# Optimization experiments

Measured on AMD Instinct MI355X. Metric: run time of the kernel, lower is better.

The kernel has to match this reference:

```python
import jax, jax.numpy as jnp
import numpy as np
import math

B, S, D_MODEL, H, D_LATENT = 2, 2048, 2048, 16, 512
D_HEAD = D_MODEL // H


def setup_inputs() -> dict:
    key = jax.random.key(0)
    ks = jax.random.split(key, 6)
    s = lambda fan: 1.0 / math.sqrt(fan)
    return {
        "x": jax.random.normal(ks[0], (B, S, D_MODEL), dtype=jnp.float32),
        "W_q": jax.random.normal(ks[1], (D_MODEL, D_MODEL), dtype=jnp.float32) * s(D_MODEL),
        "W_down_kv": jax.random.normal(ks[2], (D_LATENT, D_MODEL), dtype=jnp.float32) * s(D_MODEL),
        "W_up_k": jax.random.normal(ks[3], (H, D_HEAD, D_LATENT), dtype=jnp.float32) * s(D_LATENT),
        "W_up_v": jax.random.normal(ks[4], (H, D_HEAD, D_LATENT), dtype=jnp.float32) * s(D_LATENT),
        "W_o": jax.random.normal(ks[5], (D_MODEL, D_MODEL), dtype=jnp.float32) * s(D_MODEL),
    }


def reference(x, W_q, W_down_kv, W_up_k, W_up_v, W_o):
    b, s_len, d_model = x.shape
    # Q: (B, H, S, Dh)
    Q = (x @ W_q.T).reshape(b, s_len, H, D_HEAD).transpose(0, 2, 1, 3)
    # latent KV: (B, S, d_latent)
    C_kv = x @ W_down_kv.T
    # per-head up-projections fused into one einsum: (B, H, S, Dh)
    K = jnp.einsum("bsl,hdl->bhsd", C_kv, W_up_k)
    V = jnp.einsum("bsl,hdl->bhsd", C_kv, W_up_v)
    scores = jnp.einsum("bhsd,bhtd->bhst", Q, K) / math.sqrt(D_HEAD)
    attn = jax.nn.softmax(scores, axis=-1)  # dropout p=0 / eval -> identity
    out = jnp.einsum("bhst,bhtd->bhsd", attn, V)
    out = out.transpose(0, 2, 1, 3).reshape(b, s_len, H * D_HEAD)
    return out @ W_o.T
```

## Files before the change

### kernel.cpp

```cpp
#include <hip/hip_runtime.h>
#include <hip/hip_bf16.h>

typedef __hip_bfloat16 bf16;
typedef __attribute__((ext_vector_type(8))) short short8v;
typedef __attribute__((ext_vector_type(4))) short short4v;
typedef __attribute__((ext_vector_type(4))) float f32x4;

#define MFMA_16x16x32(a, b, c) __builtin_amdgcn_mfma_f32_16x16x32_bf16((a), (b), (c), 0, 0, 0)

constexpr int Bc = 2, Sc = 2048, DMc = 2048, Hc = 16, DLc = 512, DHc = 128;

__device__ __forceinline__ void gload_lds16(const bf16* g, void* lds) {
  __builtin_amdgcn_global_load_lds(
      (const __attribute__((address_space(1))) void*)g,
      (__attribute__((address_space(3))) void*)lds, 16, 0, 0);
}

__device__ __forceinline__ unsigned short bf16bits(float f) {
  return __builtin_bit_cast(unsigned short, __float2bfloat16(f));
}

struct CvtArgs {
  const float* src[6];
  bf16* dst[6];
  unsigned int cum[6];
  unsigned int total4;
};

__global__ __launch_bounds__(256) void cvt_all_kernel(CvtArgs a)
{
  unsigned int i = blockIdx.x * 256 + threadIdx.x;
  const unsigned int stride = gridDim.x * 256;
  for (; i < a.total4; i += stride) {
    int s = 0;
#pragma unroll
    for (int k = 1; k < 6; ++k) s += (i >= a.cum[k]) ? 1 : 0;
    unsigned int off = (i - a.cum[s]) * 4;
    float4 v = *(const float4*)(a.src[s] + off);
    short4v p;
    p[0] = (short)bf16bits(v.x);
    p[1] = (short)bf16bits(v.y);
    p[2] = (short)bf16bits(v.z);
    p[3] = (short)bf16bits(v.w);
    *(short4v*)(a.dst[s] + off) = p;
  }
}

template<int EPI>
__device__ __forceinline__ void gemm_tile_128(
    const bf16* __restrict__ A, const bf16* __restrict__ BT, void* __restrict__ Cv,
    int K, int ldc, int row0, int col0, bf16* As, bf16* Bs)
{
  const int tid = threadIdx.x;
  const int lane = tid & 63, wid = tid >> 6;
  const int wr = wid >> 1, wc = wid & 1;

  f32x4 acc[4][4] = {};

  const int srow = tid >> 2;
  const int scol = (tid & 3) * 8;
  const bf16* Ag = A + (size_t)(row0 + srow) * K + scol;
  const bf16* Bg = BT + (size_t)(col0 + srow) * K + scol;
  char* AsW = (char*)As + wid * 1024;
  char* BsW = (char*)Bs + wid * 1024;

  const int fr = lane & 15, fk = (lane >> 4) * 8;
  const bf16* aRd = As + (wr * 64 + fr) * 32 + fk;
  const bf16* bRd = Bs + (wc * 64 + fr) * 32 + fk;

  for (int k0 = 0; k0 < K; k0 += 32) {
    gload_lds16(Ag, AsW);
    gload_lds16(Ag + (size_t)64 * K, AsW + 4096);
    gload_lds16(Bg, BsW);
    gload_lds16(Bg + (size_t)64 * K, BsW + 4096);
    Ag += 32; Bg += 32;
    __syncthreads();
    short8v a[4], b[4];
#pragma unroll
    for (int m = 0; m < 4; ++m) a[m] = *(const short8v*)(aRd + m * 16 * 32);
#pragma unroll
    for (int n = 0; n < 4; ++n) b[n] = *(const short8v*)(bRd + n * 16 * 32);
#pragma unroll
    for (int m = 0; m < 4; ++m)
#pragma unroll
      for (int n = 0; n < 4; ++n)
        acc[m][n] = MFMA_16x16x32(a[m], b[n], acc[m][n]);
    __syncthreads();
  }

  const int crow = (lane >> 4) * 4, ccol = lane & 15;
  if (EPI == 0) {
    bf16* C = (bf16*)Cv;
#pragma unroll
    for (int m = 0; m < 4; ++m)
#pragma unroll
      for (int n = 0; n < 4; ++n) {
        bf16* Cp = C + (size_t)(row0 + wr * 64 + m * 16 + crow) * ldc
                     + col0 + wc * 64 + n * 16 + ccol;
#pragma unroll
        for (int r = 0; r < 4; ++r)
          Cp[(size_t)r * ldc] = __float2bfloat16(acc[m][n][r]);
      }
  } else if (EPI == 1) {
    bf16* C = (bf16*)Cv;
#pragma unroll
    for (int m = 0; m < 4; ++m)
#pragma unroll
      for (int n = 0; n < 4; ++n) {
        short4v pk;
#pragma unroll
        for (int r = 0; r < 4; ++r)
          pk[r] = (short)bf16bits(acc[m][n][r]);
        bf16* Cp = C + (size_t)(col0 + wc * 64 + n * 16 + ccol) * ldc
                     + row0 + wr * 64 + m * 16 + crow;
        *(short4v*)Cp = pk;
      }
  } else {
    float* C = (float*)Cv;
#pragma unroll
    for (int m = 0; m < 4; ++m)
#pragma unroll
      for (int n = 0; n < 4; ++n) {
        float* Cp = C + (size_t)(row0 + wr * 64 + m * 16 + crow) * ldc
                      + col0 + wc * 64 + n * 16 + ccol;
#pragma unroll
        for (int r = 0; r < 4; ++r)
          Cp[(size_t)r * ldc] = acc[m][n][r];
      }
  }
}

template<int EPI>
__global__ __launch_bounds__(256) void gemm_bt_kernel(
    const bf16* __restrict__ A, const bf16* __restrict__ BT, void* __restrict__ C,
    int K, int N)
{
  __shared__ bf16 As[128 * 32];
  __shared__ bf16 Bs[128 * 32];
  gemm_tile_128<EPI>(A, BT, C, K, N, blockIdx.y * 128, blockIdx.x * 128, As, Bs);
}

__global__ __launch_bounds__(256) void qkv_gemm_kernel(
    const bf16* __restrict__ xb, const bf16* __restrict__ Wqb,
    const bf16* __restrict__ Wdkvb, bf16* __restrict__ Qb, bf16* __restrict__ Ck)
{
  __shared__ bf16 As[128 * 32];
  __shared__ bf16 Bs[128 * 32];
  const int bx = blockIdx.x, row0 = blockIdx.y * 128;
  if (bx < 16)
    gemm_tile_128<0>(xb, Wqb, Qb, DMc, DMc, row0, bx * 128, As, Bs);
  else
    gemm_tile_128<0>(xb, Wdkvb, Ck, DMc, DLc, row0, (bx - 16) * 128, As, Bs);
}

__global__ __launch_bounds__(256) void up_gemm_kernel(
    const bf16* __restrict__ Ck, const bf16* __restrict__ Wukb,
    const bf16* __restrict__ Wuvb, bf16* __restrict__ Kcat, bf16* __restrict__ VTcat)
{
  __shared__ bf16 As[128 * 32];
  __shared__ bf16 Bs[128 * 32];
  const int bx = blockIdx.x, row0 = blockIdx.y * 128;
  if (bx < 16)
    gemm_tile_128<0>(Ck, Wukb, Kcat, DLc, DMc, row0, bx * 128, As, Bs);
  else
    gemm_tile_128<1>(Ck, Wuvb, VTcat, DLc, Bc * Sc, row0, (bx - 16) * 128, As, Bs);
}

constexpr int KVB = 64;
constexpr int NTT = Sc / KVB;
constexpr int VSTR = Bc * Sc;

__global__ __launch_bounds__(512, 2) void mla_attn_kernel(
    const bf16* __restrict__ Q, const bf16* __restrict__ Kcat,
    const bf16* __restrict__ VTcat, bf16* __restrict__ O)
{
  __shared__ bf16 Ks[2][KVB * DHc];
  __shared__ bf16 Vs[2][DHc * KVB];
  __shared__ bf16 Pl[8][16][64];

  const int tid = threadIdx.x, lane = tid & 63, wid = tid >> 6;
  const int h = blockIdx.y, b = blockIdx.z;
  const int q0 = blockIdx.x * 256 + wid * 32;
  const int fr = lane & 15, fg = lane >> 4;

  const bf16* Qp = Q + (size_t)(b * Sc + q0 + fr) * DMc + h * DHc + fg * 8;
  short8v qf[2][4];
#pragma unroll
  for (int mi = 0; mi < 2; ++mi)
#pragma unroll
    for (int kf = 0; kf < 4; ++kf)
      qf[mi][kf] = *(const short8v*)(Qp + (size_t)mi * 16 * DMc + kf * 32);

  const bf16* Kb = Kcat + (size_t)b * Sc * DMc + h * DHc;
  const bf16* Vb = VTcat + (size_t)(h * DHc) * VSTR + b * Sc;

  const int krow = wid * 4 + fg;
  const int kcolB = (fr * 16) ^ ((krow & 7) << 4);
  const bf16* kp = Kb + (size_t)krow * DMc + (kcolB >> 1);
  const int vrow = wid * 8 + (lane >> 3);
  const int vcolB = ((lane & 7) * 16) ^ ((lane >> 3) << 4);
  const bf16* vp = Vb + (size_t)vrow * VSTR + (vcolB >> 1);

  auto STAGE = [&](int buf) {
    char* kd = (char*)(&Ks[buf][0]) + wid * 1024;
    gload_lds16(kp, kd);
    gload_lds16(kp + (size_t)32 * DMc, kd + 8192);
    char* vd = (char*)(&Vs[buf][0]) + wid * 1024;
    gload_lds16(vp, vd);
    gload_lds16(vp + (size_t)64 * VSTR, vd + 8192);
    kp += (size_t)KVB * DMc;
    vp += KVB;
  };

  f32x4 oacc[2][8] = {};
  float m_r[2][4], l_r[2][4], msc[2][4];
#pragma unroll
  for (int mi = 0; mi < 2; ++mi)
#pragma unroll
    for (int r = 0; r < 4; ++r) {
      m_r[mi][r] = -1e30f; l_r[mi][r] = 0.f; msc[mi][r] = -1e30f;
    }
  const float SCL2 = 0.12751650f;
  const float THRraw = 47.0f;

  STAGE(0);
  int cur = 0;
  char* Pw = (char*)(&Pl[wid][0][0]);

  for (int it = 0; it < NTT; ++it) {
    asm volatile("s_waitcnt vmcnt(0)" ::: "memory");
    __builtin_amdgcn_s_barrier();
    asm volatile("" ::: "memory");
    if (it + 1 < NTT) STAGE(cur ^ 1);
    asm volatile("" ::: "memory");

    f32x4 sacc[2][4] = {};
    __builtin_amdgcn_s_setprio(1);
#pragma unroll
    for (int nf = 0; nf < 4; ++nf) {
#pragma unroll
      for (int kf = 0; kf < 4; ++kf) {
        const bf16* kr = &Ks[cur][(nf * 16 + fr) * 128 +
                                  (((kf * 64 + fg * 16) ^ ((fr & 7) << 4)) >> 1)];
        short8v kfrag = *(const short8v*)kr;
        sacc[0][nf] = MFMA_16x16x32(qf[0][kf], kfrag, sacc[0][nf]);
        sacc[1][nf] = MFMA_16x16x32(qf[1][kf], kfrag, sacc[1][nf]);
      }
    }
    __builtin_amdgcn_s_setprio(0);

    float pmax[2][4];
    float dmax = -1e30f;
#pragma unroll
    for (int mi = 0; mi < 2; ++mi)
#pragma unroll
      for (int r = 0; r < 4; ++r) {
        pmax[mi][r] = fmaxf(fmaxf(sacc[mi][0][r], sacc[mi][1][r]),
                            fmaxf(sacc[mi][2][r], sacc[mi][3][r]));
        dmax = fmaxf(dmax, pmax[mi][r] - m_r[mi][r]);
      }

    if (!__all(dmax <= THRraw)) {
#pragma unroll
      for (int mi = 0; mi < 2; ++mi) {
        f32x4 corrv;
#pragma unroll
        for (int r = 0; r < 4; ++r) {
          float red = pmax[mi][r];
#pragma unroll
          for (int mk = 1; mk < 16; mk <<= 1)
            red = fmaxf(red, __shfl_xor(red, mk, 64));
          float mnew = fmaxf(m_r[mi][r], red);
          float c = exp2f((m_r[mi][r] - mnew) * SCL2);
          m_r[mi][r] = mnew;
          msc[mi][r] = mnew * SCL2;
          l_r[mi][r] *= c;
          corrv[r] = c;
        }
#pragma unroll
        for (int df = 0; df < 8; ++df) oacc[mi][df] *= corrv;
      }
    }

    short8v pa[2][2];
#pragma unroll
    for (int mi = 0; mi < 2; ++mi) {
#pragma unroll
      for (int nf = 0; nf < 4; ++nf)
#pragma unroll
        for (int r = 0; r < 4; ++r) {
          float p = exp2f(__builtin_fmaf(sacc[mi][nf][r], SCL2, -msc[mi][r]));
          l_r[mi][r] += p;
          const int row = fg * 4 + r;
          const int cb = (nf * 32 + fr * 2) ^ ((row & 7) << 4);
          *(bf16*)(Pw + row * 128 + cb) = __float2bfloat16(p);
        }
      asm volatile("s_waitcnt lgkmcnt(0)" ::: "memory");
      __builtin_amdgcn_sched_barrier(0);
      const int rb0 = fr * 128 + ((fg * 16) ^ ((fr & 7) << 4));
      const int rb1 = fr * 128 + ((64 + fg * 16) ^ ((fr & 7) << 4));
      pa[mi][0] = *(const short8v*)(Pw + rb0);
      pa[mi][1] = *(const short8v*)(Pw + rb1);
      __builtin_amdgcn_sched_barrier(0);
    }

    __builtin_amdgcn_s_setprio(1);
#pragma unroll
    for (int tf = 0; tf < 2; ++tf) {
#pragma unroll
      for (int df = 0; df < 8; ++df) {
        const bf16* vr = &Vs[cur][(df * 16 + fr) * 64 +
                                  (((tf * 64 + fg * 16) ^ ((fr & 7) << 4)) >> 1)];
        short8v vfrag = *(const short8v*)vr;
        oacc[0][df] = MFMA_16x16x32(pa[0][tf], vfrag, oacc[0][df]);
        oacc[1][df] = MFMA_16x16x32(pa[1][tf], vfrag, oacc[1][df]);
      }
    }
    __builtin_amdgcn_s_setprio(0);

    cur ^= 1;
  }

#pragma unroll
  for (int mi = 0; mi < 2; ++mi) {
    float inv[4];
#pragma unroll
    for (int r = 0; r < 4; ++r) {
      float l = l_r[mi][r];
#pragma unroll
      for (int mk = 1; mk < 16; mk <<= 1)
        l += __shfl_xor(l, mk, 64);
      inv[r] = 1.f / l;
    }
    bf16* Op = O + (size_t)(b * Sc + q0 + mi * 16 + fg * 4) * DMc + h * DHc + fr;
#pragma unroll
    for (int df = 0; df < 8; ++df)
#pragma unroll
      for (int r = 0; r < 4; ++r)
        Op[(size_t)r * DMc + df * 16] = __float2bfloat16(oacc[mi][df][r] * inv[r]);
  }
}

extern "C" void kernel_launch(void* const* d_in, const int* in_sizes, int n_in,
                              void* d_out, int out_size, void* d_ws, size_t ws_size,
                              hipStream_t stream)
{
  const float* x    = (const float*)d_in[0];
  const float* Wq   = (const float*)d_in[1];
  const float* Wdkv = (const float*)d_in[2];
  const float* Wuk  = (const float*)d_in[3];
  const float* Wuv  = (const float*)d_in[4];
  const float* Wo   = (const float*)d_in[5];
  float* out = (float*)d_out;

  char* ws = (char*)d_ws;
  bf16* Qb    = (bf16*)(ws + 0);
  bf16* Kcat  = (bf16*)(ws + 16777216);
  bf16* VTcat = (bf16*)(ws + 33554432);
  bf16* xb    = (bf16*)(ws + 50331648);
  bf16* AO    = (bf16*)(ws + 50331648);
  bf16* Ck    = (bf16*)(ws + 67108864);
  bf16* Wqb   = (bf16*)(ws + 71303168);
  bf16* Wdkvb = (bf16*)(ws + 79691776);
  bf16* Wukb  = (bf16*)(ws + 81788928);
  bf16* Wuvb  = (bf16*)(ws + 83886080);
  bf16* Wob   = (bf16*)(ws + 85983232);

  dim3 blk(256, 1, 1);

  CvtArgs ca;
  ca.src[0] = x;    ca.dst[0] = xb;
  ca.src[1] = Wq;   ca.dst[1] = Wqb;
  ca.src[2] = Wdkv; ca.dst[2] = Wdkvb;
  ca.src[3] = Wuk;  ca.dst[3] = Wukb;
  ca.src[4] = Wuv;  ca.dst[4] = Wuvb;
  ca.src[5] = Wo;   ca.dst[5] = Wob;
  unsigned int n4[6] = { (unsigned)(Bc * Sc * DMc / 4), (unsigned)(DMc * DMc / 4),
                         (unsigned)(DLc * DMc / 4),     (unsigned)(Hc * DHc * DLc / 4),
                         (unsigned)(Hc * DHc * DLc / 4),(unsigned)(DMc * DMc / 4) };
  unsigned int acc = 0;
  for (int i = 0; i < 6; ++i) { ca.cum[i] = acc; acc += n4[i]; }
  ca.total4 = acc;
  cvt_all_kernel<<<2048, blk, 0, stream>>>(ca);

  qkv_gemm_kernel<<<dim3(20, (Bc * Sc) / 128), blk, 0, stream>>>(xb, Wqb, Wdkvb, Qb, Ck);

  up_gemm_kernel<<<dim3(32, (Bc * Sc) / 128), blk, 0, stream>>>(Ck, Wukb, Wuvb, Kcat, VTcat);

  mla_attn_kernel<<<dim3(Sc / 256, Hc, Bc), dim3(512, 1, 1), 0, stream>>>(Qb, Kcat, VTcat, AO);

  gemm_bt_kernel<2><<<dim3(DMc / 128, (Bc * Sc) / 128), blk, 0, stream>>>(AO, Wob, out, DMc, DMc);
}
```

Before: 266.6 us.

## Split attention KV range in two and merge partials in a combine kernel

```diff
diff --git a/kernel.cpp b/kernel.cpp
--- a/kernel.cpp
+++ b/kernel.cpp
@@ -18,6 +18,11 @@
 
 __device__ __forceinline__ unsigned short bf16bits(float f) {
   return __builtin_bit_cast(unsigned short, __float2bfloat16(f));
+}
+
+__device__ __forceinline__ float bf16tof(unsigned short u) {
+  unsigned int x = ((unsigned int)u) << 16;
+  return __builtin_bit_cast(float, x);
 }
 
 struct CvtArgs {
@@ -167,21 +172,29 @@
 }
 
 constexpr int KVB = 64;
-constexpr int NTT = Sc / KVB;
+constexpr int NSPL = 2;
+constexpr int NTT2 = Sc / NSPL / KVB;
 constexpr int VSTR = Bc * Sc;
 
-__global__ __launch_bounds__(512, 2) void mla_attn_kernel(
+__global__ __launch_bounds__(512, 4) void mla_attn_kernel(
     const bf16* __restrict__ Q, const bf16* __restrict__ Kcat,
-    const bf16* __restrict__ VTcat, bf16* __restrict__ O)
+    const bf16* __restrict__ VTcat,
+    bf16* __restrict__ Op0, bf16* __restrict__ Op1,
+    float* __restrict__ ml0, float* __restrict__ ml1)
 {
   __shared__ bf16 Ks[2][KVB * DHc];
   __shared__ bf16 Vs[2][DHc * KVB];
   __shared__ bf16 Pl[8][16][64];
 
   const int tid = threadIdx.x, lane = tid & 63, wid = tid >> 6;
-  const int h = blockIdx.y, b = blockIdx.z;
+  const int h = blockIdx.y;
+  const int b = blockIdx.z >> 1, spl = blockIdx.z & 1;
   const int q0 = blockIdx.x * 256 + wid * 32;
   const int fr = lane & 15, fg = lane >> 4;
+  const int tbase = spl * (Sc / NSPL);
+
+  bf16* Po = spl ? Op1 : Op0;
+  float* mlp = spl ? ml1 : ml0;
 
   const bf16* Qp = Q + (size_t)(b * Sc + q0 + fr) * DMc + h * DHc + fg * 8;
   short8v qf[2][4];
@@ -196,10 +209,10 @@
 
   const int krow = wid * 4 + fg;
   const int kcolB = (fr * 16) ^ ((krow & 7) << 4);
-  const bf16* kp = Kb + (size_t)krow * DMc + (kcolB >> 1);
+  const bf16* kp = Kb + (size_t)(krow + tbase) * DMc + (kcolB >> 1);
   const int vrow = wid * 8 + (lane >> 3);
   const int vcolB = ((lane & 7) * 16) ^ ((lane >> 3) << 4);
-  const bf16* vp = Vb + (size_t)vrow * VSTR + (vcolB >> 1);
+  const bf16* vp = Vb + (size_t)vrow * VSTR + (vcolB >> 1) + tbase;
 
   auto STAGE = [&](int buf) {
     char* kd = (char*)(&Ks[buf][0]) + wid * 1024;
@@ -227,11 +240,11 @@
   int cur = 0;
   char* Pw = (char*)(&Pl[wid][0][0]);
 
-  for (int it = 0; it < NTT; ++it) {
+  for (int it = 0; it < NTT2; ++it) {
     asm volatile("s_waitcnt vmcnt(0)" ::: "memory");
     __builtin_amdgcn_s_barrier();
     asm volatile("" ::: "memory");
-    if (it + 1 < NTT) STAGE(cur ^ 1);
+    if (it + 1 < NTT2) STAGE(cur ^ 1);
     asm volatile("" ::: "memory");
 
     f32x4 sacc[2][4] = {};
@@ -323,22 +336,58 @@
 
 #pragma unroll
   for (int mi = 0; mi < 2; ++mi) {
-    float inv[4];
+    float lred[4];
 #pragma unroll
     for (int r = 0; r < 4; ++r) {
       float l = l_r[mi][r];
 #pragma unroll
       for (int mk = 1; mk < 16; mk <<= 1)
         l += __shfl_xor(l, mk, 64);
-      inv[r] = 1.f / l;
-    }
-    bf16* Op = O + (size_t)(b * Sc + q0 + mi * 16 + fg * 4) * DMc + h * DHc + fr;
+      lred[r] = l;
+    }
+    if (fr == 0) {
+#pragma unroll
+      for (int r = 0; r < 4; ++r) {
+        int idx = (b * Hc + h) * Sc + q0 + mi * 16 + fg * 4 + r;
+        *(float2*)(mlp + 2 * idx) = make_float2(m_r[mi][r], lred[r]);
+      }
+    }
+    bf16* Pp = Po + (size_t)(b * Sc + q0 + mi * 16 + fg * 4) * DMc + h * DHc + fr;
 #pragma unroll
     for (int df = 0; df < 8; ++df)
 #pragma unroll
       for (int r = 0; r < 4; ++r)
-        Op[(size_t)r * DMc + df * 16] = __float2bfloat16(oacc[mi][df][r] * inv[r]);
-  }
+        Pp[(size_t)r * DMc + df * 16] = __float2bfloat16(oacc[mi][df][r]);
+  }
+}
+
+__global__ __launch_bounds__(256) void attn_combine_kernel(
+    const bf16* __restrict__ Op0, const bf16* __restrict__ Op1,
+    const float* __restrict__ ml0, const float* __restrict__ ml1,
+    bf16* __restrict__ AO)
+{
+  const float SCL2 = 0.12751650f;
+  int idx = blockIdx.x * 256 + threadIdx.x;
+  int col8 = idx & (DMc / 8 - 1);
+  int row = idx >> 8;
+  int h = col8 >> 4;
+  int b = row >> 11, q = row & (Sc - 1);
+  int mlIdx = ((b * Hc + h) * Sc + q) * 2;
+  float m0 = ml0[mlIdx], l0 = ml0[mlIdx + 1];
+  float m1 = ml1[mlIdx], l1 = ml1[mlIdx + 1];
+  float M = fmaxf(m0, m1);
+  float w0 = exp2f((m0 - M) * SCL2), w1 = exp2f((m1 - M) * SCL2);
+  float inv = 1.f / (w0 * l0 + w1 * l1);
+  w0 *= inv; w1 *= inv;
+  short8v a0 = *(const short8v*)(Op0 + (size_t)idx * 8);
+  short8v a1 = *(const short8v*)(Op1 + (size_t)idx * 8);
+  short8v o;
+#pragma unroll
+  for (int j = 0; j < 8; ++j) {
+    float v = w0 * bf16tof((unsigned short)a0[j]) + w1 * bf16tof((unsigned short)a1[j]);
+    o[j] = (short)bf16bits(v);
+  }
+  *(short8v*)(AO + (size_t)idx * 8) = o;
 }
 
 extern "C" void kernel_launch(void* const* d_in, const int* in_sizes, int n_in,
@@ -358,12 +407,16 @@
   bf16* Kcat  = (bf16*)(ws + 16777216);
   bf16* VTcat = (bf16*)(ws + 33554432);
   bf16* xb    = (bf16*)(ws + 50331648);
+  bf16* Op0   = (bf16*)(ws + 50331648);
   bf16* AO    = (bf16*)(ws + 50331648);
   bf16* Ck    = (bf16*)(ws + 67108864);
+  bf16* Op1   = (bf16*)(ws + 67108864);
   bf16* Wqb   = (bf16*)(ws + 71303168);
   bf16* Wdkvb = (bf16*)(ws + 79691776);
   bf16* Wukb  = (bf16*)(ws + 81788928);
   bf16* Wuvb  = (bf16*)(ws + 83886080);
+  float* ml0  = (float*)(ws + 83886080);
+  float* ml1  = (float*)(ws + 84410368);
   bf16* Wob   = (bf16*)(ws + 85983232);
 
   dim3 blk(256, 1, 1);
@@ -387,7 +440,11 @@
 
   up_gemm_kernel<<<dim3(32, (Bc * Sc) / 128), blk, 0, stream>>>(Ck, Wukb, Wuvb, Kcat, VTcat);
 
-  mla_attn_kernel<<<dim3(Sc / 256, Hc, Bc), dim3(512, 1, 1), 0, stream>>>(Qb, Kcat, VTcat, AO);
+  mla_attn_kernel<<<dim3(Sc / 256, Hc, Bc * NSPL), dim3(512, 1, 1), 0, stream>>>(
+      Qb, Kcat, VTcat, Op0, Op1, ml0, ml1);
+
+  attn_combine_kernel<<<dim3((Bc * Sc * DMc / 8) / 256), blk, 0, stream>>>(
+      Op0, Op1, ml0, ml1, AO);
 
   gemm_bt_kernel<2><<<dim3(DMc / 128, (Bc * Sc) / 128), blk, 0, stream>>>(AO, Wob, out, DMc, DMc);
 }
```

New measurement: 637.6 us. 2.39x slower.

## Transpose QK^T MFMA so each lane owns one query row in softmax

Applied to the files above, without the earlier changes.

```diff
diff --git a/kernel.cpp b/kernel.cpp
--- a/kernel.cpp
+++ b/kernel.cpp
@@ -176,7 +176,7 @@
 {
   __shared__ bf16 Ks[2][KVB * DHc];
   __shared__ bf16 Vs[2][DHc * KVB];
-  __shared__ bf16 Pl[8][16][64];
+  __shared__ bf16 Pl[8 * 2 * 1024];
 
   const int tid = threadIdx.x, lane = tid & 63, wid = tid >> 6;
   const int h = blockIdx.y, b = blockIdx.z;
@@ -213,19 +213,16 @@
   };
 
   f32x4 oacc[2][8] = {};
-  float m_r[2][4], l_r[2][4], msc[2][4];
-#pragma unroll
-  for (int mi = 0; mi < 2; ++mi)
-#pragma unroll
-    for (int r = 0; r < 4; ++r) {
-      m_r[mi][r] = -1e30f; l_r[mi][r] = 0.f; msc[mi][r] = -1e30f;
-    }
+  float m_r[2], l_r[2], msc[2];
+#pragma unroll
+  for (int mi = 0; mi < 2; ++mi) { m_r[mi] = -1e30f; l_r[mi] = 0.f; msc[mi] = 0.f; }
   const float SCL2 = 0.12751650f;
   const float THRraw = 47.0f;
 
   STAGE(0);
   int cur = 0;
-  char* Pw = (char*)(&Pl[wid][0][0]);
+  char* Pb = (char*)Pl + wid * 4096;
+  const int swz = (fr & 7) << 4;
 
   for (int it = 0; it < NTT; ++it) {
     asm volatile("s_waitcnt vmcnt(0)" ::: "memory");
@@ -243,66 +240,73 @@
         const bf16* kr = &Ks[cur][(nf * 16 + fr) * 128 +
                                   (((kf * 64 + fg * 16) ^ ((fr & 7) << 4)) >> 1)];
         short8v kfrag = *(const short8v*)kr;
-        sacc[0][nf] = MFMA_16x16x32(qf[0][kf], kfrag, sacc[0][nf]);
-        sacc[1][nf] = MFMA_16x16x32(qf[1][kf], kfrag, sacc[1][nf]);
+        sacc[0][nf] = MFMA_16x16x32(kfrag, qf[0][kf], sacc[0][nf]);
+        sacc[1][nf] = MFMA_16x16x32(kfrag, qf[1][kf], sacc[1][nf]);
       }
     }
     __builtin_amdgcn_s_setprio(0);
 
-    float pmax[2][4];
+    float pml[2];
     float dmax = -1e30f;
 #pragma unroll
+    for (int mi = 0; mi < 2; ++mi) {
+      float pm = sacc[mi][0][0];
+#pragma unroll
+      for (int nf = 0; nf < 4; ++nf)
+#pragma unroll
+        for (int r = 0; r < 4; ++r)
+          pm = fmaxf(pm, sacc[mi][nf][r]);
+      pml[mi] = pm;
+      dmax = fmaxf(dmax, pm - m_r[mi]);
+    }
+
+    if (!__all(dmax <= THRraw)) {
+#pragma unroll
+      for (int mi = 0; mi < 2; ++mi) {
+        float red = pml[mi];
+        red = fmaxf(red, __shfl_xor(red, 16, 64));
+        red = fmaxf(red, __shfl_xor(red, 32, 64));
+        float mnew = fmaxf(m_r[mi], red);
+        float c = exp2f((m_r[mi] - mnew) * SCL2);
+        m_r[mi] = mnew;
+        msc[mi] = mnew * SCL2;
+        l_r[mi] *= c;
+        f32x4 cv;
+#pragma unroll
+        for (int r = 0; r < 4; ++r) cv[r] = __shfl(c, fg * 4 + r, 64);
+#pragma unroll
+        for (int df = 0; df < 8; ++df) oacc[mi][df] *= cv;
+      }
+    }
+
+#pragma unroll
+    for (int mi = 0; mi < 2; ++mi) {
+      char* Pm = Pb + mi * 2048;
+#pragma unroll
+      for (int nf = 0; nf < 4; ++nf) {
+        float p0 = exp2f(__builtin_fmaf(sacc[mi][nf][0], SCL2, -msc[mi]));
+        float p1 = exp2f(__builtin_fmaf(sacc[mi][nf][1], SCL2, -msc[mi]));
+        float p2 = exp2f(__builtin_fmaf(sacc[mi][nf][2], SCL2, -msc[mi]));
+        float p3 = exp2f(__builtin_fmaf(sacc[mi][nf][3], SCL2, -msc[mi]));
+        l_r[mi] += (p0 + p1) + (p2 + p3);
+        uint2 w;
+        w.x = (unsigned)bf16bits(p0) | ((unsigned)bf16bits(p1) << 16);
+        w.y = (unsigned)bf16bits(p2) | ((unsigned)bf16bits(p3) << 16);
+        *(uint2*)(Pm + fr * 128 + ((nf * 32 + fg * 8) ^ swz)) = w;
+      }
+    }
+
+    asm volatile("s_waitcnt lgkmcnt(0)" ::: "memory");
+    __builtin_amdgcn_sched_barrier(0);
+
+    short8v pa[2][2];
+#pragma unroll
     for (int mi = 0; mi < 2; ++mi)
 #pragma unroll
-      for (int r = 0; r < 4; ++r) {
-        pmax[mi][r] = fmaxf(fmaxf(sacc[mi][0][r], sacc[mi][1][r]),
-                            fmaxf(sacc[mi][2][r], sacc[mi][3][r]));
-        dmax = fmaxf(dmax, pmax[mi][r] - m_r[mi][r]);
-      }
-
-    if (!__all(dmax <= THRraw)) {
-#pragma unroll
-      for (int mi = 0; mi < 2; ++mi) {
-        f32x4 corrv;
-#pragma unroll
-        for (int r = 0; r < 4; ++r) {
-          float red = pmax[mi][r];
-#pragma unroll
-          for (int mk = 1; mk < 16; mk <<= 1)
-            red = fmaxf(red, __shfl_xor(red, mk, 64));
-          float mnew = fmaxf(m_r[mi][r], red);
-          float c = exp2f((m_r[mi][r] - mnew) * SCL2);
-          m_r[mi][r] = mnew;
-          msc[mi][r] = mnew * SCL2;
-          l_r[mi][r] *= c;
-          corrv[r] = c;
-        }
-#pragma unroll
-        for (int df = 0; df < 8; ++df) oacc[mi][df] *= corrv;
-      }
-    }
-
-    short8v pa[2][2];
-#pragma unroll
-    for (int mi = 0; mi < 2; ++mi) {
-#pragma unroll
-      for (int nf = 0; nf < 4; ++nf)
-#pragma unroll
-        for (int r = 0; r < 4; ++r) {
-          float p = exp2f(__builtin_fmaf(sacc[mi][nf][r], SCL2, -msc[mi][r]));
-          l_r[mi][r] += p;
-          const int row = fg * 4 + r;
-          const int cb = (nf * 32 + fr * 2) ^ ((row & 7) << 4);
-          *(bf16*)(Pw + row * 128 + cb) = __float2bfloat16(p);
-        }
-      asm volatile("s_waitcnt lgkmcnt(0)" ::: "memory");
-      __builtin_amdgcn_sched_barrier(0);
-      const int rb0 = fr * 128 + ((fg * 16) ^ ((fr & 7) << 4));
-      const int rb1 = fr * 128 + ((64 + fg * 16) ^ ((fr & 7) << 4));
-      pa[mi][0] = *(const short8v*)(Pw + rb0);
-      pa[mi][1] = *(const short8v*)(Pw + rb1);
-      __builtin_amdgcn_sched_barrier(0);
-    }
+      for (int tf = 0; tf < 2; ++tf)
+        pa[mi][tf] = *(const short8v*)(Pb + mi * 2048 + fr * 128 +
+                                       ((tf * 64 + fg * 16) ^ swz));
+    __builtin_amdgcn_sched_barrier(0);
 
     __builtin_amdgcn_s_setprio(1);
 #pragma unroll
@@ -323,21 +327,19 @@
 
 #pragma unroll
   for (int mi = 0; mi < 2; ++mi) {
-    float inv[4];
-#pragma unroll
-    for (int r = 0; r < 4; ++r) {
-      float l = l_r[mi][r];
-#pragma unroll
-      for (int mk = 1; mk < 16; mk <<= 1)
-        l += __shfl_xor(l, mk, 64);
-      inv[r] = 1.f / l;
-    }
+    float l = l_r[mi];
+    l += __shfl_xor(l, 16, 64);
+    l += __shfl_xor(l, 32, 64);
+    float inv = 1.f / l;
+    f32x4 iv;
+#pragma unroll
+    for (int r = 0; r < 4; ++r) iv[r] = __shfl(inv, fg * 4 + r, 64);
     bf16* Op = O + (size_t)(b * Sc + q0 + mi * 16 + fg * 4) * DMc + h * DHc + fr;
 #pragma unroll
     for (int df = 0; df < 8; ++df)
 #pragma unroll
       for (int r = 0; r < 4; ++r)
-        Op[(size_t)r * DMc + df * 16] = __float2bfloat16(oacc[mi][df][r] * inv[r]);
+        Op[(size_t)r * DMc + df * 16] = __float2bfloat16(oacc[mi][df][r] * iv[r]);
   }
 }
 
@@ -387,7 +389,8 @@
 
   up_gemm_kernel<<<dim3(32, (Bc * Sc) / 128), blk, 0, stream>>>(Ck, Wukb, Wuvb, Kcat, VTcat);
 
-  mla_attn_kernel<<<dim3(Sc / 256, Hc, Bc), dim3(512, 1, 1), 0, stream>>>(Qb, Kcat, VTcat, AO);
+  mla_attn_kernel<<<dim3(Sc / 256, Hc, Bc), dim3(512, 1, 1), 0, stream>>>(
+      Qb, Kcat, VTcat, AO);
 
   gemm_bt_kernel<2><<<dim3(DMc / 128, (Bc * Sc) / 128), blk, 0, stream>>>(AO, Wob, out, DMc, DMc);
 }
```

Measured after the change: 258.0 us. 3.2% less time.
